# Performance work log

Hardware: AMD Instinct MI355X
Metric: run time of the kernel (lower is better)

The kernel has to match this reference:

```python
import jax, jax.numpy as jnp
import numpy as np

B, S_BERT, L_WORD, D = 64, 512, 256, 768
REDUC, HID, TAGS, POL = 400, 100, 5, 4


def _make_positions():
    # Each word spans 1-2 consecutive subwords; 256 words * max 2 <= 512 subwords.
    rng = np.random.default_rng(0)
    lens = rng.integers(1, 3, size=(B, L_WORD))          # [B, L] in {1,2}
    starts = np.cumsum(lens, axis=1) - lens              # exclusive prefix sum
    ends = starts + lens - 1                             # inclusive end, <= 511
    return jnp.asarray(np.stack([starts, ends], axis=-1), dtype=jnp.int32)


def setup_inputs() -> dict:
    key = jax.random.key(0)
    ks = jax.random.split(key, 8)
    s = 0.02
    return {
        "bert_vectors": jax.random.normal(ks[0], (B, S_BERT, D), jnp.float32),
        "positions": _make_positions(),
        "W_reduc": jax.random.normal(ks[1], (D, REDUC), jnp.float32) * s,
        "b_reduc": jnp.zeros((REDUC,), jnp.float32),
        "W_ap": jax.random.normal(ks[2], (REDUC, HID), jnp.float32) * s,
        "b_ap": jnp.zeros((HID,), jnp.float32),
        "W_op": jax.random.normal(ks[3], (REDUC, HID), jnp.float32) * s,
        "b_op": jnp.zeros((HID,), jnp.float32),
        "W_ap_tag": jax.random.normal(ks[4], (HID, TAGS), jnp.float32) * s,
        "b_ap_tag": jnp.zeros((TAGS,), jnp.float32),
        "W_op_tag": jax.random.normal(ks[5], (HID, TAGS), jnp.float32) * s,
        "b_op_tag": jnp.zeros((TAGS,), jnp.float32),
        # Biaffine: bias=(True, False) -> in1 gets a ones column: [HID+1, POL*HID]
        "W_bi": jax.random.normal(ks[6], (HID + 1, POL * HID), jnp.float32) * s,
    }


def _segment_mean(vectors, positions):
    # vectors: [B, S, D]; positions: [B, L, 2] inclusive (start, end) spans.
    cs = jnp.cumsum(vectors, axis=1)
    cs = jnp.concatenate([jnp.zeros_like(cs[:, :1]), cs], axis=1)   # [B, S+1, D]
    starts = positions[..., 0]
    ends = positions[..., 1]
    hi = jnp.take_along_axis(cs, (ends + 1)[..., None], axis=1)     # [B, L, D]
    lo = jnp.take_along_axis(cs, starts[..., None], axis=1)
    lens = (ends - starts + 1).astype(vectors.dtype)[..., None]
    return (hi - lo) / lens                                          # [B, L, D]


def reference(bert_vectors, positions, W_reduc, b_reduc, W_ap, b_ap, W_op, b_op,
              W_ap_tag, b_ap_tag, W_op_tag, b_op_tag, W_bi):
    pooled = _segment_mean(bert_vectors, positions)                  # [B, L, D]
    h = jax.nn.relu(pooled @ W_reduc + b_reduc)                      # [B, L, 400]
    ap = jax.nn.relu(h @ W_ap + b_ap)                                # [B, L, 100]
    op = jax.nn.relu(h @ W_op + b_op)                                # [B, L, 100]
    ap_out = ap @ W_ap_tag + b_ap_tag                                # [B, L, T]
    op_out = op @ W_op_tag + b_op_tag                                # [B, L, T]
    # Biaffine with bias=(True, False)
    ones = jnp.ones_like(ap[..., :1])
    a1 = jnp.concatenate([ap, ones], axis=-1)                        # [B, L, 101]
    affine = (a1 @ W_bi).reshape(ap.shape[0], ap.shape[1], POL, HID) # [B, L1, P, H]
    triplet = jnp.einsum('biph,bjh->bjip', affine, op)               # [B, L2, L1, P]
    return ap_out, op_out, triplet
```

## Files before the change

### kernel.cpp

```cpp
#include <hip/hip_runtime.h>
#include <hip/hip_bf16.h>

#define B_    64
#define S_    512
#define L_    256
#define D_    768
#define RED_  400
#define REDP_ 512
#define HID_  100
#define HIDP_ 128
#define TAGS_ 5
#define POL_  4
#define NBI_  512
#define NAO_  256
#define BL_   (B_ * L_)

typedef __attribute__((ext_vector_type(8))) short short8;
typedef __attribute__((ext_vector_type(4))) float f32x4;
typedef __attribute__((ext_vector_type(4))) unsigned short u16x4;

#define GLOAD_LDS16(gp, lp) __builtin_amdgcn_global_load_lds( \
    (const __attribute__((address_space(1))) void*)(gp),      \
    (__attribute__((address_space(3))) void*)(lp), 16, 0, 0)

__device__ inline float bf2f(unsigned short u) {
    union { unsigned int i; float f; } c; c.i = ((unsigned)u) << 16; return c.f;
}
__device__ inline unsigned short f2bf(float f) {
    __hip_bfloat16 h = __float2bfloat16(f);
    unsigned short u;
    __builtin_memcpy(&u, &h, 2);
    return u;
}

#define SZ0 393216
#define SZ1 131072
#define SZ2 65536
#define SZ3 512
#define SZ4 256
#define PREP_TOT (SZ0 + SZ1 + SZ2 + SZ3 + SZ4)

__global__ __launch_bounds__(256) void prep_kernel(
    const float* __restrict__ W_reduc, const float* __restrict__ b_reduc,
    const float* __restrict__ W_ap, const float* __restrict__ b_ap,
    const float* __restrict__ W_op, const float* __restrict__ b_op,
    const float* __restrict__ W_bi,
    unsigned short* __restrict__ WtR, unsigned short* __restrict__ WtAO,
    unsigned short* __restrict__ WtBi,
    float* __restrict__ bR, float* __restrict__ bAO, float* __restrict__ bBi)
{
    int idx = blockIdx.x * 256 + threadIdx.x;
    if (idx < SZ0) {
        int n = idx / D_, k = idx - n * D_;
        float v = (n < RED_) ? W_reduc[(size_t)k * RED_ + n] : 0.f;
        WtR[idx] = f2bf(v);
    } else if (idx < SZ0 + SZ1) {
        int i = idx - SZ0;
        int n = i >> 9, k = i & 511;
        float v = 0.f;
        if (k < RED_) {
            if (n < HID_)                      v = W_ap[(size_t)k * HID_ + n];
            else if (n >= 128 && n < 128+HID_) v = W_op[(size_t)k * HID_ + (n-128)];
        }
        WtAO[i] = f2bf(v);
    } else if (idx < SZ0 + SZ1 + SZ2) {
        int i = idx - SZ0 - SZ1;
        int n = i >> 7, k = i & 127;
        int p = n >> 7, h = n & 127;
        float v = (h < HID_ && k < HID_) ? W_bi[(size_t)k * RED_ + p * HID_ + h] : 0.f;
        WtBi[i] = f2bf(v);
        if (k == 0) bBi[n] = (h < HID_) ? W_bi[(size_t)HID_ * RED_ + p * HID_ + h] : 0.f;
    } else if (idx < SZ0 + SZ1 + SZ2 + SZ3) {
        int n = idx - SZ0 - SZ1 - SZ2;
        bR[n] = (n < RED_) ? b_reduc[n] : 0.f;
    } else if (idx < PREP_TOT) {
        int n = idx - SZ0 - SZ1 - SZ2 - SZ3;
        bAO[n] = (n < 128) ? ((n < HID_) ? b_ap[n] : 0.f)
                           : (((n-128) < HID_) ? b_op[n-128] : 0.f);
    }
}

__global__ __launch_bounds__(256) void seg_mean_kernel(
    const float* __restrict__ bert, const int* __restrict__ pos,
    unsigned short* __restrict__ pooled)
{
    int r  = threadIdx.x >> 6;
    int l  = threadIdx.x & 63;
    int bl = blockIdx.x * 4 + r;
    int b  = bl >> 8;
    int s  = pos[bl * 2 + 0];
    int e  = pos[bl * 2 + 1];
    int len = e - s + 1;
    const float* v0 = bert + ((size_t)b * S_ + s) * D_;
    float inv = (len == 2) ? 0.5f : 1.0f;
    unsigned short* outp = pooled + (size_t)bl * D_;
    #pragma unroll
    for (int c = 0; c < 3; ++c) {
        int d = l * 4 + c * 256;
        f32x4 x = *(const f32x4*)(v0 + d);
        if (len == 2) {
            f32x4 y = *(const f32x4*)(v0 + D_ + d);
            x += y;
        }
        u16x4 o;
        #pragma unroll
        for (int j = 0; j < 4; ++j) o[j] = f2bf(x[j] * inv);
        *(u16x4*)(outp + d) = o;
    }
}

template <bool RELU, bool SPLIT>
__global__ __launch_bounds__(256) void gemm_mfma_kernel(
    const short* __restrict__ A, const short* __restrict__ Bt,
    const float* __restrict__ bias, void* __restrict__ Cout,
    void* __restrict__ Cout2, int M, int N, int K)
{
    __shared__ __align__(16) short lds[2][8192];

    const int t  = threadIdx.x;
    const int wv = t >> 6;
    const int ln = t & 63;
    const int wm = wv >> 1;
    const int wn = wv & 1;
    const int bm = blockIdx.x * 128;
    const int bn = blockIdx.y * 128;

    const int srow = t >> 2;
    const int skc  = (t & 3) * 8;

    f32x4 acc[4][4] = {};

    const int NT = K >> 5;

    {
        #pragma unroll
        for (int q = 0; q < 2; ++q) {
            const short* g = A + (size_t)(bm + q * 64 + srow) * K + skc;
            GLOAD_LDS16(g, &lds[0][q * 2048 + wv * 512]);
        }
        #pragma unroll
        for (int q = 0; q < 2; ++q) {
            const short* g = Bt + (size_t)(bn + q * 64 + srow) * K + skc;
            GLOAD_LDS16(g, &lds[0][4096 + q * 2048 + wv * 512]);
        }
    }
    __syncthreads();

    int cur = 0;
    const int lr = ln & 15;
    const int lk = (ln >> 4) * 8;

    for (int kt = 0; kt < NT; ++kt) {
        if (kt + 1 < NT) {
            int k0 = (kt + 1) << 5;
            #pragma unroll
            for (int q = 0; q < 2; ++q) {
                const short* g = A + (size_t)(bm + q * 64 + srow) * K + k0 + skc;
                GLOAD_LDS16(g, &lds[cur ^ 1][q * 2048 + wv * 512]);
            }
            #pragma unroll
            for (int q = 0; q < 2; ++q) {
                const short* g = Bt + (size_t)(bn + q * 64 + srow) * K + k0 + skc;
                GLOAD_LDS16(g, &lds[cur ^ 1][4096 + q * 2048 + wv * 512]);
            }
        }

        const short* As = &lds[cur][0];
        const short* Bs = &lds[cur][4096];
        short8 a[4], b[4];
        #pragma unroll
        for (int fi = 0; fi < 4; ++fi)
            a[fi] = *(const short8*)(As + (wm * 64 + fi * 16 + lr) * 32 + lk);
        #pragma unroll
        for (int fj = 0; fj < 4; ++fj)
            b[fj] = *(const short8*)(Bs + (wn * 64 + fj * 16 + lr) * 32 + lk);
        #pragma unroll
        for (int fi = 0; fi < 4; ++fi)
            #pragma unroll
            for (int fj = 0; fj < 4; ++fj)
                acc[fi][fj] = __builtin_amdgcn_mfma_f32_16x16x32_bf16(
                    a[fi], b[fj], acc[fi][fj], 0, 0, 0);

        __syncthreads();
        cur ^= 1;
    }

    const int row0    = bm + wm * 64 + (ln >> 4) * 4;
    const int colloc0 = wn * 64 + lr;
    if (SPLIT) {
        unsigned short* Co = (unsigned short*)(bn ? Cout2 : Cout);
        #pragma unroll
        for (int fi = 0; fi < 4; ++fi)
            #pragma unroll
            for (int r = 0; r < 4; ++r) {
                int row = row0 + fi * 16 + r;
                #pragma unroll
                for (int fj = 0; fj < 4; ++fj) {
                    int cl = colloc0 + fj * 16;
                    float v = acc[fi][fj][r] + bias[bn + cl];
                    if (RELU) v = fmaxf(v, 0.f);
                    Co[(size_t)row * 128 + cl] = f2bf(v);
                }
            }
    } else {
        unsigned short* Co = (unsigned short*)Cout;
        #pragma unroll
        for (int fi = 0; fi < 4; ++fi)
            #pragma unroll
            for (int r = 0; r < 4; ++r) {
                int row = row0 + fi * 16 + r;
                #pragma unroll
                for (int fj = 0; fj < 4; ++fj) {
                    int col = bn + colloc0 + fj * 16;
                    float v = acc[fi][fj][r] + bias[col];
                    if (RELU) v = fmaxf(v, 0.f);
                    Co[(size_t)row * N + col] = f2bf(v);
                }
            }
    }
}

__global__ __launch_bounds__(256) void triplet_mfma_kernel(
    const short* __restrict__ op, const short* __restrict__ affine,
    float* __restrict__ out)
{
    __shared__ __align__(16) short lds[2][8192];

    const int t  = threadIdx.x;
    const int wv = t >> 6;
    const int ln = t & 63;
    const int wm = wv >> 1;
    const int wn = wv & 1;
    const int bm = blockIdx.x * 128;
    const int bn = blockIdx.y * 128;
    const int b  = blockIdx.z;

    const short* Ab = op     + (size_t)b * 256 * HIDP_;
    const short* Bb = affine + (size_t)b * 256 * NBI_;

    const int srow = t >> 2;
    const int skc  = (t & 3) * 8;

    f32x4 acc[4][4] = {};

    {
        #pragma unroll
        for (int q = 0; q < 2; ++q) {
            const short* g = Ab + (size_t)(bm + q * 64 + srow) * HIDP_ + skc;
            GLOAD_LDS16(g, &lds[0][q * 2048 + wv * 512]);
        }
        #pragma unroll
        for (int q = 0; q < 2; ++q) {
            int ip = bn + q * 64 + srow;
            const short* g = Bb + (size_t)(ip >> 2) * NBI_ + (ip & 3) * HIDP_ + skc;
            GLOAD_LDS16(g, &lds[0][4096 + q * 2048 + wv * 512]);
        }
    }
    __syncthreads();

    int cur = 0;
    const int lr = ln & 15;
    const int lk = (ln >> 4) * 8;

    #pragma unroll
    for (int kt = 0; kt < 4; ++kt) {
        if (kt + 1 < 4) {
            int k0 = (kt + 1) << 5;
            #pragma unroll
            for (int q = 0; q < 2; ++q) {
                const short* g = Ab + (size_t)(bm + q * 64 + srow) * HIDP_ + k0 + skc;
                GLOAD_LDS16(g, &lds[cur ^ 1][q * 2048 + wv * 512]);
            }
            #pragma unroll
            for (int q = 0; q < 2; ++q) {
                int ip = bn + q * 64 + srow;
                const short* g = Bb + (size_t)(ip >> 2) * NBI_ + (ip & 3) * HIDP_ + k0 + skc;
                GLOAD_LDS16(g, &lds[cur ^ 1][4096 + q * 2048 + wv * 512]);
            }
        }

        const short* As = &lds[cur][0];
        const short* Bs = &lds[cur][4096];
        short8 a[4], bf[4];
        #pragma unroll
        for (int fi = 0; fi < 4; ++fi)
            a[fi] = *(const short8*)(As + (wm * 64 + fi * 16 + lr) * 32 + lk);
        #pragma unroll
        for (int fj = 0; fj < 4; ++fj)
            bf[fj] = *(const short8*)(Bs + (wn * 64 + fj * 16 + lr) * 32 + lk);
        #pragma unroll
        for (int fi = 0; fi < 4; ++fi)
            #pragma unroll
            for (int fj = 0; fj < 4; ++fj)
                acc[fi][fj] = __builtin_amdgcn_mfma_f32_16x16x32_bf16(
                    a[fi], bf[fj], acc[fi][fj], 0, 0, 0);

        __syncthreads();
        cur ^= 1;
    }

    float* O = out + (size_t)b * 256 * 1024;
    const int row0 = bm + wm * 64 + (ln >> 4) * 4;
    const int col0 = bn + wn * 64 + lr;
    #pragma unroll
    for (int fi = 0; fi < 4; ++fi)
        #pragma unroll
        for (int r = 0; r < 4; ++r) {
            int row = row0 + fi * 16 + r;
            #pragma unroll
            for (int fj = 0; fj < 4; ++fj)
                O[(size_t)row * 1024 + col0 + fj * 16] = acc[fi][fj][r];
        }
}

__global__ __launch_bounds__(256) void tag_kernel(
    const short* __restrict__ ap, const short* __restrict__ op,
    const float* __restrict__ Wap, const float* __restrict__ bap,
    const float* __restrict__ Wop, const float* __restrict__ bop,
    float* __restrict__ out)
{
    __shared__ float Wl[2][HID_][TAGS_];
    __shared__ float bl[2][TAGS_];
    int t = threadIdx.x;
    for (int i = t; i < HID_ * TAGS_; i += 256) {
        Wl[0][i / TAGS_][i % TAGS_] = Wap[i];
        Wl[1][i / TAGS_][i % TAGS_] = Wop[i];
    }
    if (t < TAGS_) { bl[0][t] = bap[t]; bl[1][t] = bop[t]; }
    __syncthreads();

    int row = blockIdx.x * 256 + t;
    #pragma unroll
    for (int half = 0; half < 2; ++half) {
        const short* x = (half ? op : ap) + (size_t)row * HIDP_;
        float s[TAGS_];
        #pragma unroll
        for (int g = 0; g < TAGS_; ++g) s[g] = bl[half][g];
        #pragma unroll
        for (int c = 0; c < 12; ++c) {
            short8 v = *(const short8*)(x + c * 8);
            #pragma unroll
            for (int j = 0; j < 8; ++j) {
                float xv = bf2f((unsigned short)v[j]);
                int k = c * 8 + j;
                #pragma unroll
                for (int g = 0; g < TAGS_; ++g) s[g] += xv * Wl[half][k][g];
            }
        }
        #pragma unroll
        for (int k = 96; k < HID_; ++k) {
            float xv = bf2f(*(const unsigned short*)(x + k));
            #pragma unroll
            for (int g = 0; g < TAGS_; ++g) s[g] += xv * Wl[half][k][g];
        }
        float* o = out + (size_t)half * (BL_ * TAGS_) + (size_t)row * TAGS_;
        #pragma unroll
        for (int g = 0; g < TAGS_; ++g) o[g] = s[g];
    }
}

extern "C" void kernel_launch(void* const* d_in, const int* in_sizes, int n_in,
                              void* d_out, int out_size, void* d_ws, size_t ws_size,
                              hipStream_t stream)
{
    const float* bert     = (const float*)d_in[0];
    const int*   pos      = (const int*)  d_in[1];
    const float* W_reduc  = (const float*)d_in[2];
    const float* b_reduc  = (const float*)d_in[3];
    const float* W_ap     = (const float*)d_in[4];
    const float* b_ap     = (const float*)d_in[5];
    const float* W_op     = (const float*)d_in[6];
    const float* b_op     = (const float*)d_in[7];
    const float* W_ap_tag = (const float*)d_in[8];
    const float* b_ap_tag = (const float*)d_in[9];
    const float* W_op_tag = (const float*)d_in[10];
    const float* b_op_tag = (const float*)d_in[11];
    const float* W_bi     = (const float*)d_in[12];

    float* out = (float*)d_out;

    char* ws = (char*)d_ws;
    unsigned short* pooled = (unsigned short*)ws; ws += (size_t)BL_ * D_ * 2;
    unsigned short* h      = (unsigned short*)ws; ws += (size_t)BL_ * REDP_ * 2;
    unsigned short* ap     = (unsigned short*)ws; ws += (size_t)BL_ * HIDP_ * 2;
    unsigned short* opv    = (unsigned short*)ws; ws += (size_t)BL_ * HIDP_ * 2;
    unsigned short* affine = (unsigned short*)ws; ws += (size_t)BL_ * NBI_ * 2;
    unsigned short* WtR    = (unsigned short*)ws; ws += (size_t)REDP_ * D_ * 2;
    unsigned short* WtAO   = (unsigned short*)ws; ws += (size_t)NAO_ * REDP_ * 2;
    unsigned short* WtBi   = (unsigned short*)ws; ws += (size_t)NBI_ * HIDP_ * 2;
    float* bR  = (float*)ws;  ws += REDP_ * 4;
    float* bAO = (float*)ws;  ws += NAO_ * 4;
    float* bBi = (float*)ws;  ws += NBI_ * 4;

    prep_kernel<<<(PREP_TOT + 255) / 256, 256, 0, stream>>>(
        W_reduc, b_reduc, W_ap, b_ap, W_op, b_op, W_bi,
        WtR, WtAO, WtBi, bR, bAO, bBi);

    seg_mean_kernel<<<BL_ / 4, 256, 0, stream>>>(bert, pos, pooled);

    gemm_mfma_kernel<true, false><<<dim3(BL_ / 128, REDP_ / 128), 256, 0, stream>>>(
        (const short*)pooled, (const short*)WtR, bR, h, nullptr, BL_, REDP_, D_);

    gemm_mfma_kernel<true, true><<<dim3(BL_ / 128, NAO_ / 128), 256, 0, stream>>>(
        (const short*)h, (const short*)WtAO, bAO, ap, opv, BL_, NAO_, REDP_);

    gemm_mfma_kernel<false, false><<<dim3(BL_ / 128, NBI_ / 128), 256, 0, stream>>>(
        (const short*)ap, (const short*)WtBi, bBi, affine, nullptr, BL_, NBI_, HIDP_);

    tag_kernel<<<BL_ / 256, 256, 0, stream>>>(
        (const short*)ap, (const short*)opv,
        W_ap_tag, b_ap_tag, W_op_tag, b_op_tag, out);

    triplet_mfma_kernel<<<dim3(2, 8, B_), 256, 0, stream>>>(
        (const short*)opv, (const short*)affine, out + 2 * BL_ * TAGS_);
}
```

Before: 95.04 us.

## Fuse prep with segment mean, tag head into GEMM epilogue, single-stage K loads

Merges the weight-prep and segment-mean kernels into one launch, and fuses the tag projection into the ap/op GEMM epilogue through an fp32 LDS tile, removing the separate tag kernel and its reread of ap/op. The K=128 affine and triplet GEMMs now load the whole K extent into LDS at once, dropping the double-buffer loop and its per-step barriers. Together this cuts two launches and some global traffic, at the cost of much larger LDS use per block (about 64 KB for the small GEMMs and roughly 84 KB in the fused tag kernel), which may lower occupancy. The tag head now uses the unrounded fp32 activations rather than bf16 values.

After: 84.50 us. -11.1%, faster.

```diff
diff --git a/kernel.cpp b/kernel.cpp
--- a/kernel.cpp
+++ b/kernel.cpp
@@ -39,8 +39,12 @@
 #define SZ3 512
 #define SZ4 256
 #define PREP_TOT (SZ0 + SZ1 + SZ2 + SZ3 + SZ4)
-
-__global__ __launch_bounds__(256) void prep_kernel(
+#define SEG_BLOCKS (BL_ / 4)
+#define PREP_BLOCKS ((PREP_TOT + 255) / 256)
+
+__global__ __launch_bounds__(256) void front_kernel(
+    const float* __restrict__ bert, const int* __restrict__ pos,
+    unsigned short* __restrict__ pooled,
     const float* __restrict__ W_reduc, const float* __restrict__ b_reduc,
     const float* __restrict__ W_ap, const float* __restrict__ b_ap,
     const float* __restrict__ W_op, const float* __restrict__ b_op,
@@ -49,7 +53,34 @@
     unsigned short* __restrict__ WtBi,
     float* __restrict__ bR, float* __restrict__ bAO, float* __restrict__ bBi)
 {
-    int idx = blockIdx.x * 256 + threadIdx.x;
+    if (blockIdx.x < SEG_BLOCKS) {
+        int r  = threadIdx.x >> 6;
+        int l  = threadIdx.x & 63;
+        int bl = blockIdx.x * 4 + r;
+        int b  = bl >> 8;
+        int s  = pos[bl * 2 + 0];
+        int e  = pos[bl * 2 + 1];
+        int len = e - s + 1;
+        const float* v0 = bert + ((size_t)b * S_ + s) * D_;
+        float inv = (len == 2) ? 0.5f : 1.0f;
+        unsigned short* outp = pooled + (size_t)bl * D_;
+        #pragma unroll
+        for (int c = 0; c < 3; ++c) {
+            int d = l * 4 + c * 256;
+            f32x4 x = *(const f32x4*)(v0 + d);
+            if (len == 2) {
+                f32x4 y = *(const f32x4*)(v0 + D_ + d);
+                x += y;
+            }
+            u16x4 o;
+            #pragma unroll
+            for (int j = 0; j < 4; ++j) o[j] = f2bf(x[j] * inv);
+            *(u16x4*)(outp + d) = o;
+        }
+        return;
+    }
+
+    int idx = (blockIdx.x - SEG_BLOCKS) * 256 + threadIdx.x;
     if (idx < SZ0) {
         int n = idx / D_, k = idx - n * D_;
         float v = (n < RED_) ? W_reduc[(size_t)k * RED_ + n] : 0.f;
@@ -80,40 +111,10 @@
     }
 }
 
-__global__ __launch_bounds__(256) void seg_mean_kernel(
-    const float* __restrict__ bert, const int* __restrict__ pos,
-    unsigned short* __restrict__ pooled)
-{
-    int r  = threadIdx.x >> 6;
-    int l  = threadIdx.x & 63;
-    int bl = blockIdx.x * 4 + r;
-    int b  = bl >> 8;
-    int s  = pos[bl * 2 + 0];
-    int e  = pos[bl * 2 + 1];
-    int len = e - s + 1;
-    const float* v0 = bert + ((size_t)b * S_ + s) * D_;
-    float inv = (len == 2) ? 0.5f : 1.0f;
-    unsigned short* outp = pooled + (size_t)bl * D_;
-    #pragma unroll
-    for (int c = 0; c < 3; ++c) {
-        int d = l * 4 + c * 256;
-        f32x4 x = *(const f32x4*)(v0 + d);
-        if (len == 2) {
-            f32x4 y = *(const f32x4*)(v0 + D_ + d);
-            x += y;
-        }
-        u16x4 o;
-        #pragma unroll
-        for (int j = 0; j < 4; ++j) o[j] = f2bf(x[j] * inv);
-        *(u16x4*)(outp + d) = o;
-    }
-}
-
-template <bool RELU, bool SPLIT>
-__global__ __launch_bounds__(256) void gemm_mfma_kernel(
+__global__ __launch_bounds__(256) void gemm1_kernel(
     const short* __restrict__ A, const short* __restrict__ Bt,
-    const float* __restrict__ bias, void* __restrict__ Cout,
-    void* __restrict__ Cout2, int M, int N, int K)
+    const float* __restrict__ bias, unsigned short* __restrict__ Co,
+    int M, int N, int K)
 {
     __shared__ __align__(16) short lds[2][8192];
 
@@ -129,7 +130,6 @@
     const int skc  = (t & 3) * 8;
 
     f32x4 acc[4][4] = {};
-
     const int NT = K >> 5;
 
     {
@@ -185,46 +185,213 @@
         cur ^= 1;
     }
 
-    const int row0    = bm + wm * 64 + (ln >> 4) * 4;
-    const int colloc0 = wn * 64 + lr;
-    if (SPLIT) {
-        unsigned short* Co = (unsigned short*)(bn ? Cout2 : Cout);
-        #pragma unroll
-        for (int fi = 0; fi < 4; ++fi)
-            #pragma unroll
-            for (int r = 0; r < 4; ++r) {
-                int row = row0 + fi * 16 + r;
-                #pragma unroll
-                for (int fj = 0; fj < 4; ++fj) {
-                    int cl = colloc0 + fj * 16;
-                    float v = acc[fi][fj][r] + bias[bn + cl];
-                    if (RELU) v = fmaxf(v, 0.f);
-                    Co[(size_t)row * 128 + cl] = f2bf(v);
-                }
-            }
-    } else {
-        unsigned short* Co = (unsigned short*)Cout;
-        #pragma unroll
-        for (int fi = 0; fi < 4; ++fi)
-            #pragma unroll
-            for (int r = 0; r < 4; ++r) {
-                int row = row0 + fi * 16 + r;
-                #pragma unroll
-                for (int fj = 0; fj < 4; ++fj) {
-                    int col = bn + colloc0 + fj * 16;
-                    float v = acc[fi][fj][r] + bias[col];
-                    if (RELU) v = fmaxf(v, 0.f);
-                    Co[(size_t)row * N + col] = f2bf(v);
-                }
-            }
-    }
-}
-
-__global__ __launch_bounds__(256) void triplet_mfma_kernel(
+    const int row0 = bm + wm * 64 + (ln >> 4) * 4;
+    const int col0 = bn + wn * 64 + lr;
+    #pragma unroll
+    for (int fi = 0; fi < 4; ++fi)
+        #pragma unroll
+        for (int r = 0; r < 4; ++r) {
+            int row = row0 + fi * 16 + r;
+            #pragma unroll
+            for (int fj = 0; fj < 4; ++fj) {
+                int col = col0 + fj * 16;
+                float v = fmaxf(acc[fi][fj][r] + bias[col], 0.f);
+                Co[(size_t)row * N + col] = f2bf(v);
+            }
+        }
+}
+
+__global__ __launch_bounds__(256) void gemm23_tag_kernel(
+    const short* __restrict__ A, const short* __restrict__ Bt,
+    const float* __restrict__ bias,
+    unsigned short* __restrict__ apOut, unsigned short* __restrict__ opOut,
+    const float* __restrict__ Wap_tag, const float* __restrict__ bap_tag,
+    const float* __restrict__ Wop_tag, const float* __restrict__ bop_tag,
+    float* __restrict__ out_tag)
+{
+    __shared__ __align__(16) short lds[2][8192];
+    __shared__ float tagf[128 * 101];
+    __shared__ float Wtag[HID_ * TAGS_];
+    __shared__ float Btag[TAGS_];
+
+    const int t  = threadIdx.x;
+    const int wv = t >> 6;
+    const int ln = t & 63;
+    const int wm = wv >> 1;
+    const int wn = wv & 1;
+    const int bm = blockIdx.x * 128;
+    const int bn = blockIdx.y * 128;
+    const int half = blockIdx.y;
+
+    const float* Wt = half ? Wop_tag : Wap_tag;
+    const float* bt = half ? bop_tag : bap_tag;
+    for (int i = t; i < HID_ * TAGS_; i += 256) Wtag[i] = Wt[i];
+    if (t < TAGS_) Btag[t] = bt[t];
+
+    const int srow = t >> 2;
+    const int skc  = (t & 3) * 8;
+    const int K = REDP_;
+
+    f32x4 acc[4][4] = {};
+
+    {
+        #pragma unroll
+        for (int q = 0; q < 2; ++q) {
+            const short* g = A + (size_t)(bm + q * 64 + srow) * K + skc;
+            GLOAD_LDS16(g, &lds[0][q * 2048 + wv * 512]);
+        }
+        #pragma unroll
+        for (int q = 0; q < 2; ++q) {
+            const short* g = Bt + (size_t)(bn + q * 64 + srow) * K + skc;
+            GLOAD_LDS16(g, &lds[0][4096 + q * 2048 + wv * 512]);
+        }
+    }
+    __syncthreads();
+
+    int cur = 0;
+    const int lr = ln & 15;
+    const int lk = (ln >> 4) * 8;
+
+    for (int kt = 0; kt < 16; ++kt) {
+        if (kt + 1 < 16) {
+            int k0 = (kt + 1) << 5;
+            #pragma unroll
+            for (int q = 0; q < 2; ++q) {
+                const short* g = A + (size_t)(bm + q * 64 + srow) * K + k0 + skc;
+                GLOAD_LDS16(g, &lds[cur ^ 1][q * 2048 + wv * 512]);
+            }
+            #pragma unroll
+            for (int q = 0; q < 2; ++q) {
+                const short* g = Bt + (size_t)(bn + q * 64 + srow) * K + k0 + skc;
+                GLOAD_LDS16(g, &lds[cur ^ 1][4096 + q * 2048 + wv * 512]);
+            }
+        }
+
+        const short* As = &lds[cur][0];
+        const short* Bs = &lds[cur][4096];
+        short8 a[4], b[4];
+        #pragma unroll
+        for (int fi = 0; fi < 4; ++fi)
+            a[fi] = *(const short8*)(As + (wm * 64 + fi * 16 + lr) * 32 + lk);
+        #pragma unroll
+        for (int fj = 0; fj < 4; ++fj)
+            b[fj] = *(const short8*)(Bs + (wn * 64 + fj * 16 + lr) * 32 + lk);
+        #pragma unroll
+        for (int fi = 0; fi < 4; ++fi)
+            #pragma unroll
+            for (int fj = 0; fj < 4; ++fj)
+                acc[fi][fj] = __builtin_amdgcn_mfma_f32_16x16x32_bf16(
+                    a[fi], b[fj], acc[fi][fj], 0, 0, 0);
+
+        __syncthreads();
+        cur ^= 1;
+    }
+
+    unsigned short* Co = half ? opOut : apOut;
+    const int rl0 = wm * 64 + (ln >> 4) * 4;
+    const int cl0 = wn * 64 + lr;
+    #pragma unroll
+    for (int fi = 0; fi < 4; ++fi)
+        #pragma unroll
+        for (int r = 0; r < 4; ++r) {
+            int rl = rl0 + fi * 16 + r;
+            #pragma unroll
+            for (int fj = 0; fj < 4; ++fj) {
+                int cl = cl0 + fj * 16;
+                float v = fmaxf(acc[fi][fj][r] + bias[bn + cl], 0.f);
+                Co[(size_t)(bm + rl) * 128 + cl] = f2bf(v);
+                if (cl < 101) tagf[rl * 101 + cl] = v;
+            }
+        }
+    __syncthreads();
+
+    if (t < 128) {
+        float s[TAGS_];
+        #pragma unroll
+        for (int g = 0; g < TAGS_; ++g) s[g] = Btag[g];
+        const float* rowp = &tagf[t * 101];
+        for (int k = 0; k < HID_; ++k) {
+            float x = rowp[k];
+            #pragma unroll
+            for (int g = 0; g < TAGS_; ++g) s[g] += x * Wtag[k * TAGS_ + g];
+        }
+        float* o = out_tag + (size_t)half * (BL_ * TAGS_) + (size_t)(bm + t) * TAGS_;
+        #pragma unroll
+        for (int g = 0; g < TAGS_; ++g) o[g] = s[g];
+    }
+}
+
+__global__ __launch_bounds__(256) void affine_kernel(
+    const short* __restrict__ ap, const short* __restrict__ WtBi,
+    const float* __restrict__ bBi, unsigned short* __restrict__ affine)
+{
+    __shared__ __align__(16) short As[16384];
+    __shared__ __align__(16) short Bs[16384];
+
+    const int t  = threadIdx.x;
+    const int wv = t >> 6;
+    const int ln = t & 63;
+    const int wm = wv >> 1;
+    const int wn = wv & 1;
+    const int bm = blockIdx.x * 128;
+    const int bn = blockIdx.y * 128;
+
+    const int rsub = ln >> 2;
+    const int j8   = (ln & 3) * 8;
+
+    #pragma unroll
+    for (int i = 0; i < 8; ++i) {
+        int ks = i >> 1, hf = i & 1;
+        int rloc = wv * 32 + hf * 16;
+        const short* gA = ap + (size_t)(bm + rloc + rsub) * HIDP_ + ks * 32 + j8;
+        GLOAD_LDS16(gA, &As[ks * 4096 + rloc * 32]);
+        const short* gB = WtBi + (size_t)(bn + rloc + rsub) * HIDP_ + ks * 32 + j8;
+        GLOAD_LDS16(gB, &Bs[ks * 4096 + rloc * 32]);
+    }
+    __syncthreads();
+
+    const int lr = ln & 15;
+    const int lk = (ln >> 4) * 8;
+    f32x4 acc[4][4] = {};
+
+    #pragma unroll
+    for (int ks = 0; ks < 4; ++ks) {
+        short8 a[4], b[4];
+        #pragma unroll
+        for (int fi = 0; fi < 4; ++fi)
+            a[fi] = *(const short8*)(As + ks * 4096 + (wm * 64 + fi * 16 + lr) * 32 + lk);
+        #pragma unroll
+        for (int fj = 0; fj < 4; ++fj)
+            b[fj] = *(const short8*)(Bs + ks * 4096 + (wn * 64 + fj * 16 + lr) * 32 + lk);
+        #pragma unroll
+        for (int fi = 0; fi < 4; ++fi)
+            #pragma unroll
+            for (int fj = 0; fj < 4; ++fj)
+                acc[fi][fj] = __builtin_amdgcn_mfma_f32_16x16x32_bf16(
+                    a[fi], b[fj], acc[fi][fj], 0, 0, 0);
+    }
+
+    const int row0 = bm + wm * 64 + (ln >> 4) * 4;
+    const int col0 = bn + wn * 64 + lr;
+    #pragma unroll
+    for (int fi = 0; fi < 4; ++fi)
+        #pragma unroll
+        for (int r = 0; r < 4; ++r) {
+            int row = row0 + fi * 16 + r;
+            #pragma unroll
+            for (int fj = 0; fj < 4; ++fj) {
+                int col = col0 + fj * 16;
+                affine[(size_t)row * NBI_ + col] = f2bf(acc[fi][fj][r] + bBi[col]);
+            }
+        }
+}
+
+__global__ __launch_bounds__(256) void triplet_kernel(
     const short* __restrict__ op, const short* __restrict__ affine,
     float* __restrict__ out)
 {
-    __shared__ __align__(16) short lds[2][8192];
+    __shared__ __align__(16) short As[16384];
+    __shared__ __align__(16) short Bs[16384];
 
     const int t  = threadIdx.x;
     const int wv = t >> 6;
@@ -238,65 +405,40 @@
     const short* Ab = op     + (size_t)b * 256 * HIDP_;
     const short* Bb = affine + (size_t)b * 256 * NBI_;
 
-    const int srow = t >> 2;
-    const int skc  = (t & 3) * 8;
-
-    f32x4 acc[4][4] = {};
-
-    {
-        #pragma unroll
-        for (int q = 0; q < 2; ++q) {
-            const short* g = Ab + (size_t)(bm + q * 64 + srow) * HIDP_ + skc;
-            GLOAD_LDS16(g, &lds[0][q * 2048 + wv * 512]);
-        }
-        #pragma unroll
-        for (int q = 0; q < 2; ++q) {
-            int ip = bn + q * 64 + srow;
-            const short* g = Bb + (size_t)(ip >> 2) * NBI_ + (ip & 3) * HIDP_ + skc;
-            GLOAD_LDS16(g, &lds[0][4096 + q * 2048 + wv * 512]);
-        }
+    const int rsub = ln >> 2;
+    const int j8   = (ln & 3) * 8;
+
+    #pragma unroll
+    for (int i = 0; i < 8; ++i) {
+        int ks = i >> 1, hf = i & 1;
+        int rloc = wv * 32 + hf * 16;
+        const short* gA = Ab + (size_t)(bm + rloc + rsub) * HIDP_ + ks * 32 + j8;
+        GLOAD_LDS16(gA, &As[ks * 4096 + rloc * 32]);
+        int ip = bn + rloc + rsub;
+        const short* gB = Bb + (size_t)(ip >> 2) * NBI_ + (ip & 3) * HIDP_ + ks * 32 + j8;
+        GLOAD_LDS16(gB, &Bs[ks * 4096 + rloc * 32]);
     }
     __syncthreads();
 
-    int cur = 0;
     const int lr = ln & 15;
     const int lk = (ln >> 4) * 8;
-
-    #pragma unroll
-    for (int kt = 0; kt < 4; ++kt) {
-        if (kt + 1 < 4) {
-            int k0 = (kt + 1) << 5;
-            #pragma unroll
-            for (int q = 0; q < 2; ++q) {
-                const short* g = Ab + (size_t)(bm + q * 64 + srow) * HIDP_ + k0 + skc;
-                GLOAD_LDS16(g, &lds[cur ^ 1][q * 2048 + wv * 512]);
-            }
-            #pragma unroll
-            for (int q = 0; q < 2; ++q) {
-                int ip = bn + q * 64 + srow;
-                const short* g = Bb + (size_t)(ip >> 2) * NBI_ + (ip & 3) * HIDP_ + k0 + skc;
-                GLOAD_LDS16(g, &lds[cur ^ 1][4096 + q * 2048 + wv * 512]);
-            }
-        }
-
-        const short* As = &lds[cur][0];
-        const short* Bs = &lds[cur][4096];
+    f32x4 acc[4][4] = {};
+
+    #pragma unroll
+    for (int ks = 0; ks < 4; ++ks) {
         short8 a[4], bf[4];
         #pragma unroll
         for (int fi = 0; fi < 4; ++fi)
-            a[fi] = *(const short8*)(As + (wm * 64 + fi * 16 + lr) * 32 + lk);
+            a[fi] = *(const short8*)(As + ks * 4096 + (wm * 64 + fi * 16 + lr) * 32 + lk);
         #pragma unroll
         for (int fj = 0; fj < 4; ++fj)
-            bf[fj] = *(const short8*)(Bs + (wn * 64 + fj * 16 + lr) * 32 + lk);
+            bf[fj] = *(const short8*)(Bs + ks * 4096 + (wn * 64 + fj * 16 + lr) * 32 + lk);
         #pragma unroll
         for (int fi = 0; fi < 4; ++fi)
             #pragma unroll
             for (int fj = 0; fj < 4; ++fj)
                 acc[fi][fj] = __builtin_amdgcn_mfma_f32_16x16x32_bf16(
                     a[fi], bf[fj], acc[fi][fj], 0, 0, 0);
-
-        __syncthreads();
-        cur ^= 1;
     }
 
     float* O = out + (size_t)b * 256 * 1024;
@@ -311,52 +453,6 @@
             for (int fj = 0; fj < 4; ++fj)
                 O[(size_t)row * 1024 + col0 + fj * 16] = acc[fi][fj][r];
         }
-}
-
-__global__ __launch_bounds__(256) void tag_kernel(
-    const short* __restrict__ ap, const short* __restrict__ op,
-    const float* __restrict__ Wap, const float* __restrict__ bap,
-    const float* __restrict__ Wop, const float* __restrict__ bop,
-    float* __restrict__ out)
-{
-    __shared__ float Wl[2][HID_][TAGS_];
-    __shared__ float bl[2][TAGS_];
-    int t = threadIdx.x;
-    for (int i = t; i < HID_ * TAGS_; i += 256) {
-        Wl[0][i / TAGS_][i % TAGS_] = Wap[i];
-        Wl[1][i / TAGS_][i % TAGS_] = Wop[i];
-    }
-    if (t < TAGS_) { bl[0][t] = bap[t]; bl[1][t] = bop[t]; }
-    __syncthreads();
-
-    int row = blockIdx.x * 256 + t;
-    #pragma unroll
-    for (int half = 0; half < 2; ++half) {
-        const short* x = (half ? op : ap) + (size_t)row * HIDP_;
-        float s[TAGS_];
-        #pragma unroll
-        for (int g = 0; g < TAGS_; ++g) s[g] = bl[half][g];
-        #pragma unroll
-        for (int c = 0; c < 12; ++c) {
-            short8 v = *(const short8*)(x + c * 8);
-            #pragma unroll
-            for (int j = 0; j < 8; ++j) {
-                float xv = bf2f((unsigned short)v[j]);
-                int k = c * 8 + j;
-                #pragma unroll
-                for (int g = 0; g < TAGS_; ++g) s[g] += xv * Wl[half][k][g];
-            }
-        }
-        #pragma unroll
-        for (int k = 96; k < HID_; ++k) {
-            float xv = bf2f(*(const unsigned short*)(x + k));
-            #pragma unroll
-            for (int g = 0; g < TAGS_; ++g) s[g] += xv * Wl[half][k][g];
-        }
-        float* o = out + (size_t)half * (BL_ * TAGS_) + (size_t)row * TAGS_;
-        #pragma unroll
-        for (int g = 0; g < TAGS_; ++g) o[g] = s[g];
-    }
 }
 
 extern "C" void kernel_launch(void* const* d_in, const int* in_sizes, int n_in,
@@ -392,25 +488,21 @@
     float* bAO = (float*)ws;  ws += NAO_ * 4;
     float* bBi = (float*)ws;  ws += NBI_ * 4;
 
-    prep_kernel<<<(PREP_TOT + 255) / 256, 256, 0, stream>>>(
+    front_kernel<<<SEG_BLOCKS + PREP_BLOCKS, 256, 0, stream>>>(
+        bert, pos, pooled,
         W_reduc, b_reduc, W_ap, b_ap, W_op, b_op, W_bi,
         WtR, WtAO, WtBi, bR, bAO, bBi);
 
-    seg_mean_kernel<<<BL_ / 4, 256, 0, stream>>>(bert, pos, pooled);
-
-    gemm_mfma_kernel<true, false><<<dim3(BL_ / 128, REDP_ / 128), 256, 0, stream>>>(
-        (const short*)pooled, (const short*)WtR, bR, h, nullptr, BL_, REDP_, D_);
-
-    gemm_mfma_kernel<true, true><<<dim3(BL_ / 128, NAO_ / 128), 256, 0, stream>>>(
-        (const short*)h, (const short*)WtAO, bAO, ap, opv, BL_, NAO_, REDP_);
-
-    gemm_mfma_kernel<false, false><<<dim3(BL_ / 128, NBI_ / 128), 256, 0, stream>>>(
-        (const short*)ap, (const short*)WtBi, bBi, affine, nullptr, BL_, NBI_, HIDP_);
-
-    tag_kernel<<<BL_ / 256, 256, 0, stream>>>(
-        (const short*)ap, (const short*)opv,
+    gemm1_kernel<<<dim3(BL_ / 128, REDP_ / 128), 256, 0, stream>>>(
+        (const short*)pooled, (const short*)WtR, bR, h, BL_, REDP_, D_);
+
+    gemm23_tag_kernel<<<dim3(BL_ / 128, 2), 256, 0, stream>>>(
+        (const short*)h, (const short*)WtAO, bAO, ap, opv,
         W_ap_tag, b_ap_tag, W_op_tag, b_op_tag, out);
 
-    triplet_mfma_kernel<<<dim3(2, 8, B_), 256, 0, stream>>>(
+    affine_kernel<<<dim3(BL_ / 128, NBI_ / 128), 256, 0, stream>>>(
+        (const short*)ap, (const short*)WtBi, bBi, affine);
+
+    triplet_kernel<<<dim3(2, 8, B_), 256, 0, stream>>>(
         (const short*)opv, (const short*)affine, out + 2 * BL_ * TAGS_);
 }
```
